# Optimization experiments

Measured on AMD Instinct MI355X. Metric: run time of the kernel, lower is better.

The kernel has to match this reference:

```python
import jax, jax.numpy as jnp
import numpy as np

EPS = 1e-6

B, R, S, CSEM = 4, 16384, 48, 4


def setup_inputs() -> dict:
    key = jax.random.key(0)
    k1, k2, k3, k4, k5 = jax.random.split(key, 5)
    colors = jax.random.uniform(k1, (B, R, S, 3), dtype=jnp.float32)
    densities = jax.random.normal(k2, (B, R, S, 1), dtype=jnp.float32)
    # depths must be monotonically increasing along the sample axis
    depths = jnp.sort(jax.random.uniform(k3, (B, R, S, 1), dtype=jnp.float32) * 5.0 + 0.5, axis=2)
    # semantics: per-sample class probabilities in [0,1]
    semantics = jax.nn.softmax(jax.random.normal(k4, (B, R, S, CSEM), dtype=jnp.float32), axis=-1)
    levels = jax.random.randint(k5, (B,), 0, 3, dtype=jnp.int32)
    return {"colors": colors, "densities": densities, "depths": depths,
            "semantics": semantics, "levels": levels}


def reference(colors, densities, depths, semantics, levels):
    dtype = colors.dtype
    # midpoints along the sample axis (dim 2)
    deltas = depths[:, :, 1:] - depths[:, :, :-1]            # [B,R,S-1,1]
    colors_mid = (colors[:, :, :-1] + colors[:, :, 1:]) * 0.5
    densities_mid = (densities[:, :, :-1] + densities[:, :, 1:]) * 0.5
    depths_mid = (depths[:, :, :-1] + depths[:, :, 1:]) * 0.5
    sem_mid = (semantics[:, :, :-1] + semantics[:, :, 1:]) * 0.5

    densities_mid = jax.nn.softplus(densities_mid).astype(dtype)  # activation_factory
    alpha = 1.0 - jnp.exp(-densities_mid * deltas)                # [B,R,S-1,1]

    # per-batch level masking (vectorized version of the python loop)
    lv = levels[:, None, None, None]                              # [B,1,1,1]
    sem0 = sem_mid[..., 0:1]
    sem3 = sem_mid[..., 3:4]
    factor = jnp.where(lv == 1, 1.0 - sem0,
             jnp.where(lv == 2, 1.0 - sem0 - sem3, 1.0))
    alpha = alpha * factor

    # level 1: zero ch0, renormalize ch1..3
    tail = sem_mid[..., 1:]
    sem_l1 = jnp.concatenate(
        [jnp.zeros_like(sem0), (tail + EPS) / (tail.sum(-1, keepdims=True) + EPS)], -1)
    # level 2: zero ch0 and ch3, renormalize ch1..2
    mid2 = sem_mid[..., 1:3]
    sem_l2 = jnp.concatenate(
        [jnp.zeros_like(sem0), (mid2 + EPS) / (mid2.sum(-1, keepdims=True) + EPS),
         jnp.zeros_like(sem3)], -1)
    sem_mid = jnp.where(lv == 1, sem_l1, jnp.where(lv == 2, sem_l2, sem_mid))

    # transmittance via exclusive cumprod along sample axis
    alpha_shifted = jnp.concatenate(
        [jnp.ones_like(alpha[:, :, :1]), 1.0 - alpha + 1e-10], axis=-2)
    weights = (alpha * jnp.cumprod(alpha_shifted, axis=-2)[:, :, :-1]).astype(dtype)

    composite_rgb = jnp.sum(weights * colors_mid, axis=-2)       # [B,R,3]
    composite_depth = jnp.sum(weights * depths_mid, axis=-2)     # [B,R,1]
    composite_semantics = jnp.sum(weights * sem_mid, axis=-2)    # [B,R,CSEM]

    composite_depth = jnp.where(jnp.isnan(composite_depth), jnp.inf, composite_depth).astype(dtype)
    composite_depth = jnp.clip(composite_depth, depths.min(), depths.max())
    return composite_rgb, composite_depth, composite_semantics, weights
```

## Files before the change

kernel.cpp:

```cpp
#include <hip/hip_runtime.h>
#include <math.h>

#define EPSF 1e-6f
#define NB 4
#define NR 16384
#define NS 48
#define NSEG 47
#define NRAYS (NB * NR)
#define KL 16
#define SPL 3
#define RPT 4
#define TPB 64
#define TPBLK 8
#define NBLK (NRAYS / (RPT * TPBLK))

#define LC 0
#define LSM 576
#define LD 1344
#define LZ 1536
#define BUFSZ 1744
#define LW LC
#define LP LSM

typedef const __attribute__((address_space(1))) void as1_cvoid;
typedef __attribute__((address_space(3))) void as3_void;

__device__ __forceinline__ float softplus_f(float x) {
    return fmaxf(x, 0.0f) + __logf(1.0f + __expf(-fabsf(x)));
}

__device__ __forceinline__ void stage(const float* __restrict__ colors,
                                      const float* __restrict__ semantics,
                                      const float* __restrict__ densities,
                                      const float* __restrict__ depths,
                                      int tile, float* buf, int lane) {
    const int ray0 = tile * RPT;
    const float* c = colors + (size_t)ray0 * 144;
    __builtin_amdgcn_global_load_lds((as1_cvoid*)(c + lane * 4),
                                     (as3_void*)(buf + LC), 16, 0, 0);
    __builtin_amdgcn_global_load_lds((as1_cvoid*)(c + 256 + lane * 4),
                                     (as3_void*)(buf + LC + 256), 16, 0, 0);
    if (lane < 16)
        __builtin_amdgcn_global_load_lds((as1_cvoid*)(c + 512 + lane * 4),
                                         (as3_void*)(buf + LC + 512), 16, 0, 0);
    const float* s = semantics + (size_t)ray0 * 192;
#pragma unroll
    for (int i = 0; i < 3; ++i)
        __builtin_amdgcn_global_load_lds((as1_cvoid*)(s + i * 256 + lane * 4),
                                         (as3_void*)(buf + LSM + i * 256), 16, 0,
                                         0);
    if (lane < 48) {
        __builtin_amdgcn_global_load_lds(
            (as1_cvoid*)(densities + (size_t)ray0 * 48 + lane * 4),
            (as3_void*)(buf + LD), 16, 0, 0);
        __builtin_amdgcn_global_load_lds(
            (as1_cvoid*)(depths + (size_t)ray0 * 48 + lane * 4),
            (as3_void*)(buf + LZ), 16, 0, 0);
    }
}

__device__ __forceinline__ void do_tile(const float* lds, int tile, int lv,
                                        float* __restrict__ out, float& gmn,
                                        float& gmx, int lane, int r, int t,
                                        float* ldsw) {
    const int ray0 = tile * RPT;

    if (lane < 4) {
        gmn = fminf(gmn, lds[LZ + lane * 48]);
        gmx = fmaxf(gmx, lds[LZ + lane * 48 + 47]);
    }

    const int cb = LC + r * 144 + 9 * t;
    const float4* sp = (const float4*)(lds + LSM + r * 192);
    const int db = LD + r * 48 + 3 * t;
    const int zb = LZ + r * 48 + 3 * t;

    float pc0 = lds[cb + 0], pc1 = lds[cb + 1], pc2 = lds[cb + 2];
    float4 psm = sp[3 * t];
    float pdn = lds[db], pz = lds[zb];

    float T = 1.0f;
    float wl[SPL];
    float acc_r = 0.f, acc_g = 0.f, acc_b = 0.f, acc_d = 0.f;
    float acc_s0 = 0.f, acc_s1 = 0.f, acc_s2 = 0.f, acc_s3 = 0.f;

#pragma unroll
    for (int j = 0; j < SPL; ++j) {
        float c0 = lds[cb + 3 * (j + 1)];
        float c1 = lds[cb + 3 * (j + 1) + 1];
        float c2 = lds[cb + 3 * (j + 1) + 2];
        float4 sm4 = sp[3 * t + j + 1];
        float dn = lds[db + j + 1];
        float z = lds[zb + j + 1];

        wl[j] = 0.0f;
        if (j < 2 || t < 15) {
            float delta = z - pz;
            float cm0 = (pc0 + c0) * 0.5f;
            float cm1 = (pc1 + c1) * 0.5f;
            float cm2 = (pc2 + c2) * 0.5f;
            float dnm = (pdn + dn) * 0.5f;
            float zm = (pz + z) * 0.5f;
            float sm0 = (psm.x + sm4.x) * 0.5f;
            float sm1 = (psm.y + sm4.y) * 0.5f;
            float sm2 = (psm.z + sm4.z) * 0.5f;
            float sm3 = (psm.w + sm4.w) * 0.5f;

            float sp_ = softplus_f(dnm);
            float alpha = 1.0f - __expf(-sp_ * delta);

            float factor, o0, o1, o2, o3;
            if (lv == 1) {
                factor = 1.0f - sm0;
                float inv = 1.0f / (sm1 + sm2 + sm3 + EPSF);
                o0 = 0.0f;
                o1 = (sm1 + EPSF) * inv;
                o2 = (sm2 + EPSF) * inv;
                o3 = (sm3 + EPSF) * inv;
            } else if (lv == 2) {
                factor = 1.0f - sm0 - sm3;
                float inv = 1.0f / (sm1 + sm2 + EPSF);
                o0 = 0.0f;
                o1 = (sm1 + EPSF) * inv;
                o2 = (sm2 + EPSF) * inv;
                o3 = 0.0f;
            } else {
                factor = 1.0f;
                o0 = sm0; o1 = sm1; o2 = sm2; o3 = sm3;
            }

            alpha *= factor;
            float w = alpha * T;
            T *= (1.0f - alpha + 1e-10f);
            wl[j] = w;

            acc_r += w * cm0;
            acc_g += w * cm1;
            acc_b += w * cm2;
            acc_d += w * zm;
            acc_s0 += w * o0;
            acc_s1 += w * o1;
            acc_s2 += w * o2;
            acc_s3 += w * o3;
        }
        pc0 = c0; pc1 = c1; pc2 = c2;
        psm = sm4; pdn = dn; pz = z;
    }

    float p = T;
#pragma unroll
    for (int off = 1; off < KL; off <<= 1) {
        float u = __shfl_up(p, off, KL);
        if (t >= off) p *= u;
    }
    float Tstart = __shfl_up(p, 1, KL);
    if (t == 0) Tstart = 1.0f;

    acc_r *= Tstart; acc_g *= Tstart; acc_b *= Tstart; acc_d *= Tstart;
    acc_s0 *= Tstart; acc_s1 *= Tstart; acc_s2 *= Tstart; acc_s3 *= Tstart;

#pragma unroll
    for (int j = 0; j < SPL; ++j) {
        if (j < 2 || t < 15)
            ldsw[LW + r * NSEG + 3 * t + j] = wl[j] * Tstart;
    }

    {
        const int pb = LP + r * 144 + t * 9;
        ldsw[pb + 0] = acc_r;  ldsw[pb + 1] = acc_g;
        ldsw[pb + 2] = acc_b;  ldsw[pb + 3] = acc_d;
        ldsw[pb + 4] = acc_s0; ldsw[pb + 5] = acc_s1;
        ldsw[pb + 6] = acc_s2; ldsw[pb + 7] = acc_s3;
    }

    if (lane < 47) {
        const float4* src = (const float4*)(lds + LW);
        float4* dst = (float4*)(out + (size_t)NRAYS * 8 + (size_t)ray0 * NSEG);
        dst[lane] = src[lane];
    }

    if (lane < 32) {
        const int rr = lane >> 3, qq = lane & 7;
        const int qb = LP + rr * 144 + qq;
        float v = 0.0f;
#pragma unroll
        for (int k = 0; k < KL; ++k) v += lds[qb + 9 * k];

        const int oray = ray0 + rr;
        size_t oidx;
        if (qq < 3) {
            oidx = (size_t)oray * 3 + qq;
        } else if (qq == 3) {
            if (isnan(v)) v = INFINITY;
            oidx = (size_t)NRAYS * 3 + oray;
        } else {
            oidx = (size_t)NRAYS * 4 + (size_t)oray * 4 + (qq - 4);
        }
        out[oidx] = v;
    }
}

__global__ __launch_bounds__(TPB) void march_kernel(
    const float* __restrict__ colors, const float* __restrict__ densities,
    const float* __restrict__ depths, const float* __restrict__ semantics,
    const int* __restrict__ levels, float2* __restrict__ ws2,
    float* __restrict__ out) {
    __shared__ float lds[2 * BUFSZ];
    const int lane = threadIdx.x;
    const int r = lane >> 4;
    const int t = lane & 15;
    const int tile0 = blockIdx.x * TPBLK;
    const int lv = levels[(tile0 * RPT) >> 14];
    float gmn = INFINITY, gmx = -INFINITY;

    stage(colors, semantics, densities, depths, tile0, lds, lane);

    stage(colors, semantics, densities, depths, tile0 + 1, lds + BUFSZ, lane);
    asm volatile("" ::: "memory");
    asm volatile("s_waitcnt vmcnt(8)" ::: "memory");
    do_tile(lds, tile0, lv, out, gmn, gmx, lane, r, t, lds);

#pragma unroll 2
    for (int k = 1; k < TPBLK - 1; ++k) {
        float* nbuf = lds + (((k + 1) & 1) ? BUFSZ : 0);
        float* cbuf = lds + ((k & 1) ? BUFSZ : 0);
        stage(colors, semantics, densities, depths, tile0 + k + 1, nbuf, lane);
        asm volatile("" ::: "memory");
        asm volatile("s_waitcnt vmcnt(10)" ::: "memory");
        do_tile(cbuf, tile0 + k, lv, out, gmn, gmx, lane, r, t, cbuf);
    }

    asm volatile("s_waitcnt vmcnt(2)" ::: "memory");
    do_tile(lds + BUFSZ, tile0 + TPBLK - 1, lv, out, gmn, gmx, lane, r, t,
            lds + BUFSZ);

    gmn = fminf(gmn, __shfl_xor(gmn, 1, 4));
    gmn = fminf(gmn, __shfl_xor(gmn, 2, 4));
    gmx = fmaxf(gmx, __shfl_xor(gmx, 1, 4));
    gmx = fmaxf(gmx, __shfl_xor(gmx, 2, 4));
    if (lane == 0) ws2[blockIdx.x] = make_float2(gmn, gmx);
}

__global__ __launch_bounds__(256) void clip_depth(const float2* __restrict__ ws2,
                                                  float* __restrict__ dout) {
    __shared__ float smn[4], smx[4];
    float mn = INFINITY, mx = -INFINITY;
#pragma unroll
    for (int k = 0; k < NBLK / 256; ++k) {
        float2 v = ws2[threadIdx.x + (k << 8)];
        mn = fminf(mn, v.x);
        mx = fmaxf(mx, v.y);
    }
#pragma unroll
    for (int off = 32; off > 0; off >>= 1) {
        mn = fminf(mn, __shfl_down(mn, off));
        mx = fmaxf(mx, __shfl_down(mx, off));
    }
    if ((threadIdx.x & 63) == 0) {
        smn[threadIdx.x >> 6] = mn;
        smx[threadIdx.x >> 6] = mx;
    }
    __syncthreads();
    mn = fminf(fminf(smn[0], smn[1]), fminf(smn[2], smn[3]));
    mx = fmaxf(fmaxf(smx[0], smx[1]), fmaxf(smx[2], smx[3]));

    float4* d4 = (float4*)dout;
    const int i = blockIdx.x * 256 + threadIdx.x;
    float4 v = d4[i];
    v.x = fminf(fmaxf(v.x, mn), mx);
    v.y = fminf(fmaxf(v.y, mn), mx);
    v.z = fminf(fmaxf(v.z, mn), mx);
    v.w = fminf(fmaxf(v.w, mn), mx);
    d4[i] = v;
}

extern "C" void kernel_launch(void* const* d_in, const int* in_sizes, int n_in,
                              void* d_out, int out_size, void* d_ws, size_t ws_size,
                              hipStream_t stream) {
    const float* colors = (const float*)d_in[0];
    const float* densities = (const float*)d_in[1];
    const float* depths = (const float*)d_in[2];
    const float* semantics = (const float*)d_in[3];
    const int* levels = (const int*)d_in[4];
    float* out = (float*)d_out;
    float2* ws2 = (float2*)d_ws;

    march_kernel<<<NBLK, TPB, 0, stream>>>(colors, densities, depths, semantics,
                                           levels, ws2, out);
    clip_depth<<<64, 256, 0, stream>>>(ws2, out + (size_t)NRAYS * 3);
}
```

Baseline: 28.88 us.

## Switch to grid-stride persistent blocks with fixed block count

Replaces the fixed eight tiles per block with a grid-stride loop over tiles using a fixed grid of 2816 single-wave blocks, keeping the double-buffered LDS staging. The level index is now looked up per tile, and buffers are swapped through pointers. The aim is to balance work across CUs and cut tail effects and block launch overhead. Blocks now get an uneven tile count (16384/2816 is not whole), which can leave some imbalance. The clip_depth reduction loop over NBLK/256 still matches because 2816 is a multiple of 256.

```diff
diff --git a/kernel.cpp b/kernel.cpp
--- a/kernel.cpp
+++ b/kernel.cpp
@@ -11,8 +11,8 @@
 #define SPL 3
 #define RPT 4
 #define TPB 64
-#define TPBLK 8
-#define NBLK (NRAYS / (RPT * TPBLK))
+#define NTILES (NRAYS / RPT)
+#define NBLK 2816
 
 #define LC 0
 #define LSM 576
@@ -59,10 +59,9 @@
     }
 }
 
-__device__ __forceinline__ void do_tile(const float* lds, int tile, int lv,
+__device__ __forceinline__ void do_tile(float* lds, int tile, int lv,
                                         float* __restrict__ out, float& gmn,
-                                        float& gmx, int lane, int r, int t,
-                                        float* ldsw) {
+                                        float& gmx, int lane, int r, int t) {
     const int ray0 = tile * RPT;
 
     if (lane < 4) {
@@ -162,15 +161,15 @@
 #pragma unroll
     for (int j = 0; j < SPL; ++j) {
         if (j < 2 || t < 15)
-            ldsw[LW + r * NSEG + 3 * t + j] = wl[j] * Tstart;
+            lds[LW + r * NSEG + 3 * t + j] = wl[j] * Tstart;
     }
 
     {
         const int pb = LP + r * 144 + t * 9;
-        ldsw[pb + 0] = acc_r;  ldsw[pb + 1] = acc_g;
-        ldsw[pb + 2] = acc_b;  ldsw[pb + 3] = acc_d;
-        ldsw[pb + 4] = acc_s0; ldsw[pb + 5] = acc_s1;
-        ldsw[pb + 6] = acc_s2; ldsw[pb + 7] = acc_s3;
+        lds[pb + 0] = acc_r;  lds[pb + 1] = acc_g;
+        lds[pb + 2] = acc_b;  lds[pb + 3] = acc_d;
+        lds[pb + 4] = acc_s0; lds[pb + 5] = acc_s1;
+        lds[pb + 6] = acc_s2; lds[pb + 7] = acc_s3;
     }
 
     if (lane < 47) {
@@ -209,30 +208,33 @@
     const int lane = threadIdx.x;
     const int r = lane >> 4;
     const int t = lane & 15;
-    const int tile0 = blockIdx.x * TPBLK;
-    const int lv = levels[(tile0 * RPT) >> 14];
     float gmn = INFINITY, gmx = -INFINITY;
 
-    stage(colors, semantics, densities, depths, tile0, lds, lane);
-
-    stage(colors, semantics, densities, depths, tile0 + 1, lds + BUFSZ, lane);
+    int tile = blockIdx.x;
+    float* curb = lds;
+    float* nxtb = lds + BUFSZ;
+
+    stage(colors, semantics, densities, depths, tile, curb, lane);
+
+    int tnext = tile + NBLK;
+    stage(colors, semantics, densities, depths, tnext, nxtb, lane);
     asm volatile("" ::: "memory");
     asm volatile("s_waitcnt vmcnt(8)" ::: "memory");
-    do_tile(lds, tile0, lv, out, gmn, gmx, lane, r, t, lds);
-
-#pragma unroll 2
-    for (int k = 1; k < TPBLK - 1; ++k) {
-        float* nbuf = lds + (((k + 1) & 1) ? BUFSZ : 0);
-        float* cbuf = lds + ((k & 1) ? BUFSZ : 0);
-        stage(colors, semantics, densities, depths, tile0 + k + 1, nbuf, lane);
+    do_tile(curb, tile, levels[tile >> 12], out, gmn, gmx, lane, r, t);
+    { float* tmp = curb; curb = nxtb; nxtb = tmp; }
+    tile = tnext;
+
+    for (tnext = tile + NBLK; tnext < NTILES; tnext += NBLK) {
+        stage(colors, semantics, densities, depths, tnext, nxtb, lane);
         asm volatile("" ::: "memory");
         asm volatile("s_waitcnt vmcnt(10)" ::: "memory");
-        do_tile(cbuf, tile0 + k, lv, out, gmn, gmx, lane, r, t, cbuf);
+        do_tile(curb, tile, levels[tile >> 12], out, gmn, gmx, lane, r, t);
+        { float* tmp = curb; curb = nxtb; nxtb = tmp; }
+        tile = tnext;
     }
 
     asm volatile("s_waitcnt vmcnt(2)" ::: "memory");
-    do_tile(lds + BUFSZ, tile0 + TPBLK - 1, lv, out, gmn, gmx, lane, r, t,
-            lds + BUFSZ);
+    do_tile(curb, tile, levels[tile >> 12], out, gmn, gmx, lane, r, t);
 
     gmn = fminf(gmn, __shfl_xor(gmn, 1, 4));
     gmn = fminf(gmn, __shfl_xor(gmn, 2, 4));
```

Result: slower. 30.73 us (+6.4%).
